# Kernel optimization log

Measured on AMD Instinct MI355X. Metric: run time of the kernel, lower is better.

The kernel has to match this reference:

```python
import jax, jax.numpy as jnp
import numpy as np

B, S, D_MODEL = 2, 2048, 2048
N_HEADS, N_KV_HEADS, HEAD_DIM = 32, 8, 64
N_GROUPS = N_HEADS // N_KV_HEADS


def setup_inputs() -> dict:
    key = jax.random.key(0)
    ks = jax.random.split(key, 5)
    x = jax.random.normal(ks[0], (B, S, D_MODEL), dtype=jnp.float32)
    wq = jax.random.normal(ks[1], (N_HEADS * HEAD_DIM, D_MODEL), dtype=jnp.float32) * 0.02
    wk = jax.random.normal(ks[2], (N_KV_HEADS * HEAD_DIM, D_MODEL), dtype=jnp.float32) * 0.02
    wv = jax.random.normal(ks[3], (N_KV_HEADS * HEAD_DIM, D_MODEL), dtype=jnp.float32) * 0.02
    wo = jax.random.normal(ks[4], (D_MODEL, N_HEADS * HEAD_DIM), dtype=jnp.float32) * 0.02
    # Rotary tables: module's apply_rope expects cos/sin of shape [S, head_dim//2]
    half = HEAD_DIM // 2
    inv_freq = 1.0 / (10000.0 ** (jnp.arange(0, half, dtype=jnp.float32) / half))
    angles = jnp.arange(S, dtype=jnp.float32)[:, None] * inv_freq[None, :]  # [S, half]
    cos = jnp.cos(angles)
    sin = jnp.sin(angles)
    return {"x": x, "wq": wq, "wk": wk, "wv": wv, "wo": wo, "cos": cos, "sin": sin}


def _rotate_half(t):
    half = t.shape[-1] // 2
    return jnp.concatenate((-t[..., half:], t[..., :half]), axis=-1)


def _apply_rope(q, k, cos, sin):
    # cos/sin: [S, head_dim//2] -> repeat_interleave(2) -> [S, head_dim]
    cos2 = jnp.repeat(cos, 2, axis=-1)[None, :, None, :]  # [1,S,1,D]
    sin2 = jnp.repeat(sin, 2, axis=-1)[None, :, None, :]
    q_rot = q * cos2 + _rotate_half(q) * sin2
    k_rot = k * cos2 + _rotate_half(k) * sin2
    return q_rot, k_rot


def reference(x, wq, wk, wv, wo, cos, sin):
    b, s, _ = x.shape
    q = (x @ wq.T).reshape(b, s, N_HEADS, HEAD_DIM)
    k = (x @ wk.T).reshape(b, s, N_KV_HEADS, HEAD_DIM)
    v = (x @ wv.T).reshape(b, s, N_KV_HEADS, HEAD_DIM)
    q, k = _apply_rope(q, k, cos, sin)
    # GQA expansion: repeat_interleave along head dim
    k = jnp.repeat(k, N_GROUPS, axis=2)  # [b,s,H,D]
    v = jnp.repeat(v, N_GROUPS, axis=2)
    q = q.transpose(0, 2, 1, 3)  # [b,H,s,D]
    k = k.transpose(0, 2, 1, 3)
    v = v.transpose(0, 2, 1, 3)
    scale = HEAD_DIM ** -0.5
    scores = jnp.einsum("bhqd,bhkd->bhqk", q, k) * scale
    causal = jnp.tril(jnp.ones((s, s), dtype=bool))
    scores = jnp.where(causal[None, None], scores, jnp.finfo(scores.dtype).min)
    attn = jax.nn.softmax(scores, axis=-1)
    out = jnp.einsum("bhqk,bhkd->bhqd", attn, v)
    out = out.transpose(0, 2, 1, 3).reshape(b, s, N_HEADS * HEAD_DIM)
    return out @ wo.T
```

## Files before the change

### kernel.cpp

```cpp
#include <hip/hip_runtime.h>
#include <hip/hip_bf16.h>

#define B_   2
#define S_   2048
#define DM   2048
#define NH   32
#define NKV  8
#define HD   64
#define MROWS 4096
#define NQKV  3072

typedef __attribute__((ext_vector_type(8))) short bf16x8;
typedef __attribute__((ext_vector_type(4))) float f32x4;
typedef __attribute__((ext_vector_type(16))) float f32x16;

__device__ __forceinline__ unsigned short f2b(float f) {
  __hip_bfloat16 h = __float2bfloat16(f);
  return *reinterpret_cast<unsigned short*>(&h);
}

__device__ __forceinline__ void gload16(const void* g, void* l) {
  __builtin_amdgcn_global_load_lds((__attribute__((address_space(1))) void*)g,
                                   (__attribute__((address_space(3))) void*)l,
                                   16, 0, 0);
}

__device__ __forceinline__ unsigned cvtpk(float lo, float hi) {
  unsigned r;
  asm("v_cvt_pk_bf16_f32 %0, %1, %2" : "=v"(r) : "v"(lo), "v"(hi));
  return r;
}

__device__ __forceinline__ void pl32swap(unsigned& a, unsigned& b) {
  asm volatile("v_permlane32_swap_b32 %0, %1" : "+v"(a), "+v"(b));
}

__device__ __forceinline__ float exp2hw(float x) {
  float r;
  asm("v_exp_f32 %0, %1" : "=v"(r) : "v"(x));
  return r;
}

__device__ __forceinline__ bf16x8 mk8(unsigned w0, unsigned w1, unsigned w2, unsigned w3) {
  union { unsigned u[4]; bf16x8 v; } uu;
  uu.u[0] = w0; uu.u[1] = w1; uu.u[2] = w2; uu.u[3] = w3;
  return uu.v;
}

__global__ __launch_bounds__(256) void f2bf_kernel(const float* __restrict__ in,
                                                   unsigned short* __restrict__ out, int n4) {
  int i = blockIdx.x * 256 + threadIdx.x;
  if (i < n4) {
    float4 v = reinterpret_cast<const float4*>(in)[i];
    ushort4 o;
    o.x = f2b(v.x); o.y = f2b(v.y); o.z = f2b(v.z); o.w = f2b(v.w);
    reinterpret_cast<ushort4*>(out)[i] = o;
  }
}

__global__ __launch_bounds__(256) void wcat_kernel(const float* __restrict__ wq,
                                                   const float* __restrict__ wk,
                                                   const float* __restrict__ wv,
                                                   unsigned short* __restrict__ out) {
  int i = blockIdx.x * 256 + threadIdx.x;
  int e = i * 4;
  int row = e >> 11;
  int col = e & 2047;
  const float* src;
  if (row < 2048)      src = wq + (size_t)row * 2048 + col;
  else if (row < 2560) src = wk + (size_t)(row - 2048) * 2048 + col;
  else                 src = wv + (size_t)(row - 2560) * 2048 + col;
  float4 v = *reinterpret_cast<const float4*>(src);
  ushort4 o;
  o.x = f2b(v.x); o.y = f2b(v.y); o.z = f2b(v.z); o.w = f2b(v.w);
  reinterpret_cast<ushort4*>(out)[i] = o;
}

#define QSCALE 0.18033688011112042f

__global__ __launch_bounds__(256, 3) void gemm_qkv(const unsigned short* __restrict__ A,
                                                   const unsigned short* __restrict__ Bm,
                                                   unsigned short* __restrict__ Qb,
                                                   unsigned short* __restrict__ Kb2,
                                                   unsigned short* __restrict__ Vtb,
                                                   const float* __restrict__ cosg,
                                                   const float* __restrict__ sing) {
  const int K = DM;
  __shared__ unsigned short Abuf[3][128 * 32];
  __shared__ unsigned short Bbuf[3][128 * 32];
  const int tid = threadIdx.x;
  const int wave = tid >> 6, lane = tid & 63;
  const int wr = wave >> 1, wc = wave & 1;
  const int rowbase = blockIdx.y * 128;
  const int colbase = blockIdx.x * 128;
  const unsigned short* Ag = A + (size_t)rowbase * K;
  const unsigned short* Bg = Bm + (size_t)colbase * K;
  const int NT = K / 32;

  auto stage = [&](int buf, int k0) {
#pragma unroll
    for (int it = 0; it < 2; ++it) {
      int slot = wave * 128 + it * 64 + lane;
      int r = slot >> 2, p = slot & 3;
      gload16(Ag + (size_t)r * K + k0 + ((p ^ ((r >> 1) & 3)) << 3),
              &Abuf[buf][(wave * 128 + it * 64) * 8]);
    }
#pragma unroll
    for (int it = 0; it < 2; ++it) {
      int slot = wave * 128 + it * 64 + lane;
      int r = slot >> 2, p = slot & 3;
      gload16(Bg + (size_t)r * K + k0 + ((p ^ ((r >> 1) & 3)) << 3),
              &Bbuf[buf][(wave * 128 + it * 64) * 8]);
    }
  };
  auto ldA = [&](int buf, int row, int c) -> bf16x8 {
    return *(const bf16x8*)((const char*)&Abuf[buf][0] + row * 64 + ((c ^ ((row >> 1) & 3)) << 4));
  };
  auto ldB = [&](int buf, int row, int c) -> bf16x8 {
    return *(const bf16x8*)((const char*)&Bbuf[buf][0] + row * 64 + ((c ^ ((row >> 1) & 3)) << 4));
  };

  f32x4 acc[4][4];
#pragma unroll
  for (int a = 0; a < 4; a++)
#pragma unroll
    for (int b2 = 0; b2 < 4; b2++) acc[a][b2] = (f32x4){0.f, 0.f, 0.f, 0.f};

  const int l15 = lane & 15, l4 = lane >> 4;

  stage(0, 0);
  stage(1, 32);
  asm volatile("s_waitcnt vmcnt(4)" ::: "memory");
  __builtin_amdgcn_s_barrier();

  int cur = 0;
  for (int t = 0; t < NT; ++t) {
    const int nxt2 = (cur >= 1) ? cur - 1 : cur + 2;
    bf16x8 af[4], bfv[4];
#pragma unroll
    for (int mt = 0; mt < 4; ++mt) af[mt] = ldA(cur, wr * 64 + mt * 16 + l15, l4);
#pragma unroll
    for (int nt = 0; nt < 4; ++nt) bfv[nt] = ldB(cur, wc * 64 + nt * 16 + l15, l4);
    if (t + 2 < NT) stage(nxt2, (t + 2) * 32);
    __builtin_amdgcn_s_barrier();
    __builtin_amdgcn_s_setprio(1);
#pragma unroll
    for (int mt = 0; mt < 4; ++mt)
#pragma unroll
      for (int nt = 0; nt < 4; ++nt)
        acc[mt][nt] = __builtin_amdgcn_mfma_f32_16x16x32_bf16(af[mt], bfv[nt], acc[mt][nt], 0, 0, 0);
    __builtin_amdgcn_s_setprio(0);
    if (t < NT - 1) {
      if (t + 2 < NT) asm volatile("s_waitcnt vmcnt(4)" ::: "memory");
      else            asm volatile("s_waitcnt vmcnt(0)" ::: "memory");
      __builtin_amdgcn_s_barrier();
    }
    cur = (cur < 2) ? cur + 1 : 0;
  }

  const int orow = rowbase + wr * 64, ocol = colbase + wc * 64;
  if (colbase < 2048) {
#pragma unroll
    for (int mt = 0; mt < 4; ++mt)
#pragma unroll
      for (int r = 0; r < 4; ++r) {
        const int row = orow + mt * 16 + l4 * 4 + r;
        const int s = row & 2047;
        const float* cR = cosg + s * 32;
        const float* sR = sing + s * 32;
#pragma unroll
        for (int nt = 0; nt < 2; ++nt) {
          const int i2 = nt * 8 + (l15 >> 1);
          float c0 = cR[i2], sv0 = sR[i2], c1 = cR[16 + i2], sv1 = sR[16 + i2];
          float alo = acc[mt][nt][r], ahi = acc[mt][nt + 2][r];
          size_t base = (size_t)row * 2048 + ocol + nt * 16 + l15;
          Qb[base]      = f2b((alo * c0 - ahi * sv0) * QSCALE);
          Qb[base + 32] = f2b((ahi * c1 + alo * sv1) * QSCALE);
        }
      }
  } else if (colbase < 2560) {
    const int kcol = ocol - 2048;
#pragma unroll
    for (int mt = 0; mt < 4; ++mt)
#pragma unroll
      for (int r = 0; r < 4; ++r) {
        const int row = orow + mt * 16 + l4 * 4 + r;
        const int s = row & 2047;
        const float* cR = cosg + s * 32;
        const float* sR = sing + s * 32;
#pragma unroll
        for (int nt = 0; nt < 2; ++nt) {
          const int i2 = nt * 8 + (l15 >> 1);
          float c0 = cR[i2], sv0 = sR[i2], c1 = cR[16 + i2], sv1 = sR[16 + i2];
          float alo = acc[mt][nt][r], ahi = acc[mt][nt + 2][r];
          size_t base = (size_t)row * 512 + kcol + nt * 16 + l15;
          Kb2[base]      = f2b(alo * c0 - ahi * sv0);
          Kb2[base + 32] = f2b(ahi * c1 + alo * sv1);
        }
      }
  } else {
    const int hkv = (ocol - 2560) >> 6;
#pragma unroll
    for (int mt = 0; mt < 4; ++mt)
#pragma unroll
      for (int nt = 0; nt < 4; ++nt) {
        const int d = nt * 16 + l15;
        const int row0 = orow + mt * 16 + l4 * 4;
        const int b = row0 >> 11, s0i = row0 & 2047;
        ushort4 u;
        u.x = f2b(acc[mt][nt][0]); u.y = f2b(acc[mt][nt][1]);
        u.z = f2b(acc[mt][nt][2]); u.w = f2b(acc[mt][nt][3]);
        *(ushort4*)(Vtb + ((size_t)(b * NKV + hkv) * HD + d) * S_ + s0i) = u;
      }
  }
}

#define BMg 256
#define BNg 128
#define BKg 64
__global__ __launch_bounds__(512, 2) void gemm_bt(const unsigned short* __restrict__ A,
                                                  const unsigned short* __restrict__ Bm,
                                                  float* __restrict__ C,
                                                  int M, int N, int K) {
  __shared__ unsigned short Abuf[3][BMg * BKg];
  __shared__ unsigned short Bbuf[3][BNg * BKg];
  const int tid = threadIdx.x;
  const int wave = tid >> 6, lane = tid & 63;
  const int wr = wave >> 1, wc = wave & 1;
  const int rowbase = blockIdx.y * BMg;
  const int colbase = blockIdx.x * BNg;
  const unsigned short* Ag = A + (size_t)rowbase * K;
  const unsigned short* Bg = Bm + (size_t)colbase * K;
  const int NT = K / BKg;

  auto stage_half = [&](int buf, int k0, int half) {
#pragma unroll
    for (int i = 0; i < 2; ++i) {
      int c = wave * 256 + (half * 2 + i) * 64 + lane;
      int r = c >> 3, p = c & 7;
      gload16(Ag + (size_t)r * K + k0 + ((p ^ (r & 7)) << 3),
              &Abuf[buf][(wave * 256 + (half * 2 + i) * 64) * 8]);
    }
    int c = wave * 128 + half * 64 + lane;
    int r = c >> 3, p = c & 7;
    gload16(Bg + (size_t)r * K + k0 + ((p ^ (r & 7)) << 3),
            &Bbuf[buf][(wave * 128 + half * 64) * 8]);
  };
  auto ldA = [&](int buf, int row, int c16) -> bf16x8 {
    return *(const bf16x8*)((const char*)&Abuf[buf][0] + row * 128 + ((c16 ^ (row & 7)) << 4));
  };
  auto ldB = [&](int buf, int row, int c16) -> bf16x8 {
    return *(const bf16x8*)((const char*)&Bbuf[buf][0] + row * 128 + ((c16 ^ (row & 7)) << 4));
  };

  f32x4 acc[4][4];
#pragma unroll
  for (int a = 0; a < 4; a++)
#pragma unroll
    for (int b2 = 0; b2 < 4; b2++) acc[a][b2] = (f32x4){0.f, 0.f, 0.f, 0.f};

  const int l15 = lane & 15, l4 = lane >> 4;

  stage_half(0, 0, 0); stage_half(0, 0, 1);
  stage_half(1, BKg, 0); stage_half(1, BKg, 1);
  asm volatile("s_waitcnt vmcnt(6)" ::: "memory");
  __builtin_amdgcn_s_barrier();

  int cur = 0;
  for (int t = 0; t < NT; ++t) {
    const int nxt2 = (cur >= 1) ? cur - 1 : cur + 2;
    {
      bf16x8 af[4], bfv[4];
#pragma unroll
      for (int mt = 0; mt < 4; ++mt) af[mt] = ldA(cur, wr * 64 + mt * 16 + l15, l4);
#pragma unroll
      for (int nt = 0; nt < 4; ++nt) bfv[nt] = ldB(cur, wc * 64 + nt * 16 + l15, l4);
      if (t + 2 < NT) stage_half(nxt2, (t + 2) * BKg, 0);
      __builtin_amdgcn_s_barrier();
      __builtin_amdgcn_s_setprio(1);
#pragma unroll
      for (int mt = 0; mt < 4; ++mt)
#pragma unroll
        for (int nt = 0; nt < 4; ++nt)
          acc[mt][nt] = __builtin_amdgcn_mfma_f32_16x16x32_bf16(af[mt], bfv[nt], acc[mt][nt], 0, 0, 0);
      __builtin_amdgcn_s_setprio(0);
      __builtin_amdgcn_s_barrier();
    }
    {
      bf16x8 af[4], bfv[4];
#pragma unroll
      for (int mt = 0; mt < 4; ++mt) af[mt] = ldA(cur, wr * 64 + mt * 16 + l15, 4 + l4);
#pragma unroll
      for (int nt = 0; nt < 4; ++nt) bfv[nt] = ldB(cur, wc * 64 + nt * 16 + l15, 4 + l4);
      if (t + 2 < NT) stage_half(nxt2, (t + 2) * BKg, 1);
      __builtin_amdgcn_s_barrier();
      __builtin_amdgcn_s_setprio(1);
#pragma unroll
      for (int mt = 0; mt < 4; ++mt)
#pragma unroll
        for (int nt = 0; nt < 4; ++nt)
          acc[mt][nt] = __builtin_amdgcn_mfma_f32_16x16x32_bf16(af[mt], bfv[nt], acc[mt][nt], 0, 0, 0);
      __builtin_amdgcn_s_setprio(0);
      if (t < NT - 1) {
        if (t + 2 < NT) asm volatile("s_waitcnt vmcnt(6)" ::: "memory");
        else            asm volatile("s_waitcnt vmcnt(0)" ::: "memory");
        __builtin_amdgcn_s_barrier();
      }
    }
    cur = (cur < 2) ? cur + 1 : 0;
  }

  const int orow = rowbase + wr * 64, ocol = colbase + wc * 64;
#pragma unroll
  for (int mt = 0; mt < 4; mt++)
#pragma unroll
    for (int nt = 0; nt < 4; nt++)
#pragma unroll
      for (int r = 0; r < 4; r++)
        C[(size_t)(orow + mt * 16 + l4 * 4 + r) * N + ocol + nt * 16 + l15] = acc[mt][nt][r];
}

__global__ __launch_bounds__(256, 2) void attn_kernel(const unsigned short* __restrict__ Qb,
                                                      const unsigned short* __restrict__ Kb2,
                                                      const unsigned short* __restrict__ Vt,
                                                      unsigned short* __restrict__ AO) {
  const int pr = blockIdx.x, h = blockIdx.y, b = blockIdx.z;
  const int hk = h >> 2;
  __shared__ unsigned short Kbuf[2][8192];
  __shared__ unsigned short Vbuf[2][8192];
  const int tid = threadIdx.x, wave = tid >> 6, lane = tid & 63;
  const int l31 = lane & 31, hi = lane >> 5;

  const unsigned short* Qrow = Qb + (size_t)b * S_ * 2048 + h * 64;
  const unsigned short* Krow = Kb2 + (size_t)b * S_ * 512 + hk * 64;
  const unsigned short* Vbase = Vt + (size_t)(b * NKV + hk) * HD * S_;

  const int NT_A = 16 - pr;
  const int NTtot = 17;

  auto j0_of = [&](int tl) { return (tl < NT_A ? tl : tl - NT_A) * 128; };
  auto stage = [&](int j0, int bufi) {
#pragma unroll
    for (int it = 0; it < 4; ++it) {
      int slot = (wave * 4 + it) * 64 + lane;
      int row = slot >> 3, p = slot & 7;
      gload16(Krow + (size_t)(j0 + row) * 512 + ((p ^ (row & 7)) << 3),
              &Kbuf[bufi][(wave * 4 + it) * 512]);
    }
#pragma unroll
    for (int it = 0; it < 4; ++it) {
      int slot = (wave * 4 + it) * 64 + lane;
      int row = slot >> 4, p = slot & 15;
      gload16(Vbase + (size_t)row * S_ + j0 + ((p ^ (row & 15)) << 3),
              &Vbuf[bufi][(wave * 4 + it) * 512]);
    }
  };

  stage(j0_of(0), 0);
  stage(j0_of(1), 1);
  asm volatile("s_waitcnt vmcnt(8)" ::: "memory");
  __builtin_amdgcn_s_barrier();

  int cur = 0, tlin = 0;

  for (int rg = 0; rg < 2; ++rg) {
    const int qbi = rg == 0 ? (15 - pr) : pr;
    const int qb = qbi * 128;
    const int NT = qbi + 1;
    const int q0w = qb + wave * 32;
    const int qg = q0w + l31;

    bf16x8 qf[4];
#pragma unroll
    for (int c = 0; c < 4; ++c)
      qf[c] = *reinterpret_cast<const bf16x8*>(Qrow + (size_t)qg * 2048 + c * 16 + hi * 8);

    f32x16 Oa0 = {}, Oa1 = {};
    float m_old = -INFINITY, lsum = 0.f;

    for (int t = 0; t < NT; ++t, ++tlin) {
      const int j0 = t * 128;

      if (j0 < q0w + 32) {
        const char* Klc = (const char*)&Kbuf[cur][0];
        const char* Vlc = (const char*)&Vbuf[cur][0];

        f32x16 s0 = {}, s1 = {}, s2 = {}, s3 = {};
        __builtin_amdgcn_s_setprio(1);
#pragma unroll
        for (int c = 0; c < 4; ++c) {
          const int xb = ((c << 1) + hi) ^ (l31 & 7);
          bf16x8 kf0 = *(const bf16x8*)(Klc + (l31) * 128       + (xb << 4));
          s0 = __builtin_amdgcn_mfma_f32_32x32x16_bf16(kf0, qf[c], s0, 0, 0, 0);
          bf16x8 kf1 = *(const bf16x8*)(Klc + (32 + l31) * 128  + (xb << 4));
          s1 = __builtin_amdgcn_mfma_f32_32x32x16_bf16(kf1, qf[c], s1, 0, 0, 0);
          bf16x8 kf2 = *(const bf16x8*)(Klc + (64 + l31) * 128  + (xb << 4));
          s2 = __builtin_amdgcn_mfma_f32_32x32x16_bf16(kf2, qf[c], s2, 0, 0, 0);
          bf16x8 kf3 = *(const bf16x8*)(Klc + (96 + l31) * 128  + (xb << 4));
          s3 = __builtin_amdgcn_mfma_f32_32x32x16_bf16(kf3, qf[c], s3, 0, 0, 0);
        }
        __builtin_amdgcn_s_setprio(0);

        if (j0 + 127 > q0w) {
          const int kb0 = j0 + 4 * hi, kb1 = kb0 + 32, kb2m = kb0 + 64, kb3 = kb0 + 96;
#pragma unroll
          for (int r = 0; r < 16; ++r) {
            const int ko = (r & 3) + 8 * (r >> 2);
            if (kb0 + ko > qg) s0[r] = -INFINITY;
            if (kb1 + ko > qg) s1[r] = -INFINITY;
            if (kb2m + ko > qg) s2[r] = -INFINITY;
            if (kb3 + ko > qg) s3[r] = -INFINITY;
          }
        }

        float a0 = fmaxf(fmaxf(s0[0], s1[0]), fmaxf(s2[0], s3[0]));
        float a1 = fmaxf(fmaxf(s0[1], s1[1]), fmaxf(s2[1], s3[1]));
        float a2 = fmaxf(fmaxf(s0[2], s1[2]), fmaxf(s2[2], s3[2]));
        float a3 = fmaxf(fmaxf(s0[3], s1[3]), fmaxf(s2[3], s3[3]));
#pragma unroll
        for (int r = 4; r < 16; r += 4) {
          a0 = fmaxf(a0, fmaxf(fmaxf(s0[r], s1[r]), fmaxf(s2[r], s3[r])));
          a1 = fmaxf(a1, fmaxf(fmaxf(s0[r + 1], s1[r + 1]), fmaxf(s2[r + 1], s3[r + 1])));
          a2 = fmaxf(a2, fmaxf(fmaxf(s0[r + 2], s1[r + 2]), fmaxf(s2[r + 2], s3[r + 2])));
          a3 = fmaxf(a3, fmaxf(fmaxf(s0[r + 3], s1[r + 3]), fmaxf(s2[r + 3], s3[r + 3])));
        }
        float mxt = fmaxf(fmaxf(a0, a1), fmaxf(a2, a3));
        mxt = fmaxf(mxt, __shfl_xor(mxt, 32, 64));

        if (!__all(mxt - m_old <= 8.f)) {
          float mnew = fmaxf(m_old, mxt);
          float corr = exp2hw(m_old - mnew);
          m_old = mnew;
          lsum *= corr;
#pragma unroll
          for (int r = 0; r < 16; ++r) { Oa0[r] *= corr; Oa1[r] *= corr; }
        }

        float t0 = 0.f, t1 = 0.f, t2 = 0.f, t3 = 0.f;
#pragma unroll
        for (int r = 0; r < 16; r += 4) {
          s0[r]     = exp2hw(s0[r] - m_old);     t0 += s0[r];
          s0[r + 1] = exp2hw(s0[r + 1] - m_old); t1 += s0[r + 1];
          s0[r + 2] = exp2hw(s0[r + 2] - m_old); t2 += s0[r + 2];
          s0[r + 3] = exp2hw(s0[r + 3] - m_old); t3 += s0[r + 3];
        }
#pragma unroll
        for (int r = 0; r < 16; r += 4) {
          s1[r]     = exp2hw(s1[r] - m_old);     t0 += s1[r];
          s1[r + 1] = exp2hw(s1[r + 1] - m_old); t1 += s1[r + 1];
          s1[r + 2] = exp2hw(s1[r + 2] - m_old); t2 += s1[r + 2];
          s1[r + 3] = exp2hw(s1[r + 3] - m_old); t3 += s1[r + 3];
        }
#pragma unroll
        for (int r = 0; r < 16; r += 4) {
          s2[r]     = exp2hw(s2[r] - m_old);     t0 += s2[r];
          s2[r + 1] = exp2hw(s2[r + 1] - m_old); t1 += s2[r + 1];
          s2[r + 2] = exp2hw(s2[r + 2] - m_old); t2 += s2[r + 2];
          s2[r + 3] = exp2hw(s2[r + 3] - m_old); t3 += s2[r + 3];
        }
#pragma unroll
        for (int r = 0; r < 16; r += 4) {
          s3[r]     = exp2hw(s3[r] - m_old);     t0 += s3[r];
          s3[r + 1] = exp2hw(s3[r + 1] - m_old); t1 += s3[r + 1];
          s3[r + 2] = exp2hw(s3[r + 2] - m_old); t2 += s3[r + 2];
          s3[r + 3] = exp2hw(s3[r + 3] - m_old); t3 += s3[r + 3];
        }
        float rs = (t0 + t1) + (t2 + t3);
        rs += __shfl_xor(rs, 32, 64);
        lsum += rs;

        bf16x8 pf0, pf1, pf2, pf3, pf4, pf5, pf6, pf7;
        {
          unsigned aA = cvtpk(s0[0], s0[1]),  bA = cvtpk(s0[4], s0[5]);  pl32swap(aA, bA);
          unsigned aB = cvtpk(s0[2], s0[3]),  bB = cvtpk(s0[6], s0[7]);  pl32swap(aB, bB);
          pf0 = mk8(aA, aB, bA, bB);
          unsigned aC = cvtpk(s0[8], s0[9]),  bC = cvtpk(s0[12], s0[13]); pl32swap(aC, bC);
          unsigned aD = cvtpk(s0[10], s0[11]), bD = cvtpk(s0[14], s0[15]); pl32swap(aD, bD);
          pf1 = mk8(aC, aD, bC, bD);
        }
        {
          unsigned aA = cvtpk(s1[0], s1[1]),  bA = cvtpk(s1[4], s1[5]);  pl32swap(aA, bA);
          unsigned aB = cvtpk(s1[2], s1[3]),  bB = cvtpk(s1[6], s1[7]);  pl32swap(aB, bB);
          pf2 = mk8(aA, aB, bA, bB);
          unsigned aC = cvtpk(s1[8], s1[9]),  bC = cvtpk(s1[12], s1[13]); pl32swap(aC, bC);
          unsigned aD = cvtpk(s1[10], s1[11]), bD = cvtpk(s1[14], s1[15]); pl32swap(aD, bD);
          pf3 = mk8(aC, aD, bC, bD);
        }
        {
          unsigned aA = cvtpk(s2[0], s2[1]),  bA = cvtpk(s2[4], s2[5]);  pl32swap(aA, bA);
          unsigned aB = cvtpk(s2[2], s2[3]),  bB = cvtpk(s2[6], s2[7]);  pl32swap(aB, bB);
          pf4 = mk8(aA, aB, bA, bB);
          unsigned aC = cvtpk(s2[8], s2[9]),  bC = cvtpk(s2[12], s2[13]); pl32swap(aC, bC);
          unsigned aD = cvtpk(s2[10], s2[11]), bD = cvtpk(s2[14], s2[15]); pl32swap(aD, bD);
          pf5 = mk8(aC, aD, bC, bD);
        }
        {
          unsigned aA = cvtpk(s3[0], s3[1]),  bA = cvtpk(s3[4], s3[5]);  pl32swap(aA, bA);
          unsigned aB = cvtpk(s3[2], s3[3]),  bB = cvtpk(s3[6], s3[7]);  pl32swap(aB, bB);
          pf6 = mk8(aA, aB, bA, bB);
          unsigned aC = cvtpk(s3[8], s3[9]),  bC = cvtpk(s3[12], s3[13]); pl32swap(aC, bC);
          unsigned aD = cvtpk(s3[10], s3[11]), bD = cvtpk(s3[14], s3[15]); pl32swap(aD, bD);
          pf7 = mk8(aC, aD, bC, bD);
        }

        const int xv = l31 & 15;
        __builtin_amdgcn_s_setprio(1);
#define PVSTEP(PF, SK)                                                                     \
        {                                                                                  \
          const int xc = (((SK) << 1) + hi) ^ xv;                                          \
          bf16x8 vf0 = *(const bf16x8*)(Vlc + l31 * 256 + (xc << 4));                      \
          Oa0 = __builtin_amdgcn_mfma_f32_32x32x16_bf16(vf0, PF, Oa0, 0, 0, 0);            \
          bf16x8 vf1 = *(const bf16x8*)(Vlc + (32 + l31) * 256 + (xc << 4));               \
          Oa1 = __builtin_amdgcn_mfma_f32_32x32x16_bf16(vf1, PF, Oa1, 0, 0, 0);            \
        }
        PVSTEP(pf0, 0) PVSTEP(pf1, 1) PVSTEP(pf2, 2) PVSTEP(pf3, 3)
        PVSTEP(pf4, 4) PVSTEP(pf5, 5) PVSTEP(pf6, 6) PVSTEP(pf7, 7)
#undef PVSTEP
        __builtin_amdgcn_s_setprio(0);
      }

      __builtin_amdgcn_s_barrier();
      if (tlin + 2 < NTtot) stage(j0_of(tlin + 2), cur);
      if (tlin + 1 < NTtot) {
        if (tlin + 2 < NTtot) asm volatile("s_waitcnt vmcnt(8)" ::: "memory");
        else                  asm volatile("s_waitcnt vmcnt(0)" ::: "memory");
        __builtin_amdgcn_s_barrier();
      }
      cur ^= 1;
    }

    const float inv = 1.0f / lsum;
    unsigned short* ob = AO + (size_t)(b * S_ + qg) * 2048 + h * 64;
#pragma unroll
    for (int c = 0; c < 4; ++c) {
      ushort4 u0, u1;
      u0.x = f2b(Oa0[4 * c] * inv);     u0.y = f2b(Oa0[4 * c + 1] * inv);
      u0.z = f2b(Oa0[4 * c + 2] * inv); u0.w = f2b(Oa0[4 * c + 3] * inv);
      u1.x = f2b(Oa1[4 * c] * inv);     u1.y = f2b(Oa1[4 * c + 1] * inv);
      u1.z = f2b(Oa1[4 * c + 2] * inv); u1.w = f2b(Oa1[4 * c + 3] * inv);
      *(ushort4*)(ob + 8 * c + 4 * hi)      = u0;
      *(ushort4*)(ob + 32 + 8 * c + 4 * hi) = u1;
    }
  }
}

extern "C" void kernel_launch(void* const* d_in, const int* in_sizes, int n_in,
                              void* d_out, int out_size, void* d_ws, size_t ws_size,
                              hipStream_t stream) {
  (void)in_sizes; (void)n_in; (void)out_size; (void)ws_size;
  const float* x    = (const float*)d_in[0];
  const float* wq   = (const float*)d_in[1];
  const float* wk   = (const float*)d_in[2];
  const float* wv   = (const float*)d_in[3];
  const float* wo   = (const float*)d_in[4];
  const float* cosg = (const float*)d_in[5];
  const float* sing = (const float*)d_in[6];

  char* ws = (char*)d_ws;
  unsigned short* xb   = (unsigned short*)(ws);
  unsigned short* wcat = (unsigned short*)(ws + 16777216);
  unsigned short* wob  = (unsigned short*)(ws + 29360128);
  unsigned short* Qb   = (unsigned short*)(ws + 37748736);
  unsigned short* Kb2  = (unsigned short*)(ws + 54525952);
  unsigned short* Vtb  = (unsigned short*)(ws + 58720256);
  unsigned short* AO   = xb;

  f2bf_kernel<<<8192, 256, 0, stream>>>(x, xb, 2097152);
  wcat_kernel<<<6144, 256, 0, stream>>>(wq, wk, wv, wcat);
  f2bf_kernel<<<4096, 256, 0, stream>>>(wo, wob, 1048576);

  gemm_qkv<<<dim3(NQKV / 128, MROWS / 128), 256, 0, stream>>>(xb, wcat, Qb, Kb2, Vtb, cosg, sing);

  attn_kernel<<<dim3(8, NH, B_), 256, 0, stream>>>(Qb, Kb2, Vtb, AO);

  gemm_bt<<<dim3(DM / BNg, MROWS / BMg), 512, 0, stream>>>(AO, wob, (float*)d_out, MROWS, DM, DM);
}
```

Baseline: 184.3 us.

## Split fused QKV GEMM into a larger-tile Q GEMM and a separate KV GEMM

```diff
diff --git a/kernel.cpp b/kernel.cpp
--- a/kernel.cpp
+++ b/kernel.cpp
@@ -78,13 +78,127 @@
 
 #define QSCALE 0.18033688011112042f
 
-__global__ __launch_bounds__(256, 3) void gemm_qkv(const unsigned short* __restrict__ A,
-                                                   const unsigned short* __restrict__ Bm,
-                                                   unsigned short* __restrict__ Qb,
-                                                   unsigned short* __restrict__ Kb2,
-                                                   unsigned short* __restrict__ Vtb,
-                                                   const float* __restrict__ cosg,
-                                                   const float* __restrict__ sing) {
+__global__ __launch_bounds__(512, 2) void gemm_q(const unsigned short* __restrict__ A,
+                                                 const unsigned short* __restrict__ Bm,
+                                                 unsigned short* __restrict__ Qb,
+                                                 const float* __restrict__ cosg,
+                                                 const float* __restrict__ sing) {
+  const int K = DM;
+  __shared__ unsigned short Abuf[3][256 * 64];
+  __shared__ unsigned short Bbuf[3][128 * 64];
+  const int tid = threadIdx.x;
+  const int wave = tid >> 6, lane = tid & 63;
+  const int wr = wave >> 1, wc = wave & 1;
+  const int rowbase = blockIdx.y * 256;
+  const int colbase = blockIdx.x * 128;
+  const unsigned short* Ag = A + (size_t)rowbase * K;
+  const unsigned short* Bg = Bm + (size_t)colbase * K;
+  const int NT = K / 64;
+
+  auto stage_half = [&](int buf, int k0, int half) {
+#pragma unroll
+    for (int i = 0; i < 2; ++i) {
+      int c = wave * 256 + (half * 2 + i) * 64 + lane;
+      int r = c >> 3, p = c & 7;
+      gload16(Ag + (size_t)r * K + k0 + ((p ^ (r & 7)) << 3),
+              &Abuf[buf][(wave * 256 + (half * 2 + i) * 64) * 8]);
+    }
+    int c = wave * 128 + half * 64 + lane;
+    int r = c >> 3, p = c & 7;
+    gload16(Bg + (size_t)r * K + k0 + ((p ^ (r & 7)) << 3),
+            &Bbuf[buf][(wave * 128 + half * 64) * 8]);
+  };
+  auto ldA = [&](int buf, int row, int c16) -> bf16x8 {
+    return *(const bf16x8*)((const char*)&Abuf[buf][0] + row * 128 + ((c16 ^ (row & 7)) << 4));
+  };
+  auto ldB = [&](int buf, int row, int c16) -> bf16x8 {
+    return *(const bf16x8*)((const char*)&Bbuf[buf][0] + row * 128 + ((c16 ^ (row & 7)) << 4));
+  };
+
+  f32x4 acc[4][4];
+#pragma unroll
+  for (int a = 0; a < 4; a++)
+#pragma unroll
+    for (int b2 = 0; b2 < 4; b2++) acc[a][b2] = (f32x4){0.f, 0.f, 0.f, 0.f};
+
+  const int l15 = lane & 15, l4 = lane >> 4;
+
+  stage_half(0, 0, 0); stage_half(0, 0, 1);
+  stage_half(1, 64, 0); stage_half(1, 64, 1);
+  asm volatile("s_waitcnt vmcnt(6)" ::: "memory");
+  __builtin_amdgcn_s_barrier();
+
+  int cur = 0;
+  for (int t = 0; t < NT; ++t) {
+    const int nxt2 = (cur >= 1) ? cur - 1 : cur + 2;
+    {
+      bf16x8 af[4], bfv[4];
+#pragma unroll
+      for (int mt = 0; mt < 4; ++mt) af[mt] = ldA(cur, wr * 64 + mt * 16 + l15, l4);
+#pragma unroll
+      for (int nt = 0; nt < 4; ++nt) bfv[nt] = ldB(cur, wc * 64 + nt * 16 + l15, l4);
+      if (t + 2 < NT) stage_half(nxt2, (t + 2) * 64, 0);
+      __builtin_amdgcn_s_barrier();
+      __builtin_amdgcn_s_setprio(1);
+#pragma unroll
+      for (int mt = 0; mt < 4; ++mt)
+#pragma unroll
+        for (int nt = 0; nt < 4; ++nt)
+          acc[mt][nt] = __builtin_amdgcn_mfma_f32_16x16x32_bf16(af[mt], bfv[nt], acc[mt][nt], 0, 0, 0);
+      __builtin_amdgcn_s_setprio(0);
+      __builtin_amdgcn_s_barrier();
+    }
+    {
+      bf16x8 af[4], bfv[4];
+#pragma unroll
+      for (int mt = 0; mt < 4; ++mt) af[mt] = ldA(cur, wr * 64 + mt * 16 + l15, 4 + l4);
+#pragma unroll
+      for (int nt = 0; nt < 4; ++nt) bfv[nt] = ldB(cur, wc * 64 + nt * 16 + l15, 4 + l4);
+      if (t + 2 < NT) stage_half(nxt2, (t + 2) * 64, 1);
+      __builtin_amdgcn_s_barrier();
+      __builtin_amdgcn_s_setprio(1);
+#pragma unroll
+      for (int mt = 0; mt < 4; ++mt)
+#pragma unroll
+        for (int nt = 0; nt < 4; ++nt)
+          acc[mt][nt] = __builtin_amdgcn_mfma_f32_16x16x32_bf16(af[mt], bfv[nt], acc[mt][nt], 0, 0, 0);
+      __builtin_amdgcn_s_setprio(0);
+      if (t < NT - 1) {
+        if (t + 2 < NT) asm volatile("s_waitcnt vmcnt(6)" ::: "memory");
+        else            asm volatile("s_waitcnt vmcnt(0)" ::: "memory");
+        __builtin_amdgcn_s_barrier();
+      }
+    }
+    cur = (cur < 2) ? cur + 1 : 0;
+  }
+
+  const int orow = rowbase + wr * 64, ocol = colbase + wc * 64;
+#pragma unroll
+  for (int mt = 0; mt < 4; ++mt)
+#pragma unroll
+    for (int r = 0; r < 4; ++r) {
+      const int row = orow + mt * 16 + l4 * 4 + r;
+      const int s = row & 2047;
+      const float* cR = cosg + s * 32;
+      const float* sR = sing + s * 32;
+#pragma unroll
+      for (int nt = 0; nt < 2; ++nt) {
+        const int i2 = nt * 8 + (l15 >> 1);
+        float c0 = cR[i2], sv0 = sR[i2], c1 = cR[16 + i2], sv1 = sR[16 + i2];
+        float alo = acc[mt][nt][r], ahi = acc[mt][nt + 2][r];
+        size_t base = (size_t)row * 2048 + ocol + nt * 16 + l15;
+        Qb[base]      = f2b((alo * c0 - ahi * sv0) * QSCALE);
+        Qb[base + 32] = f2b((ahi * c1 + alo * sv1) * QSCALE);
+      }
+    }
+}
+
+__global__ __launch_bounds__(256, 3) void gemm_kv(const unsigned short* __restrict__ A,
+                                                  const unsigned short* __restrict__ Bm,
+                                                  unsigned short* __restrict__ Kb2,
+                                                  unsigned short* __restrict__ Vtb,
+                                                  const float* __restrict__ cosg,
+                                                  const float* __restrict__ sing) {
   const int K = DM;
   __shared__ unsigned short Abuf[3][128 * 32];
   __shared__ unsigned short Bbuf[3][128 * 32];
@@ -159,7 +273,7 @@
   }
 
   const int orow = rowbase + wr * 64, ocol = colbase + wc * 64;
-  if (colbase < 2048) {
+  if (colbase < 512) {
 #pragma unroll
     for (int mt = 0; mt < 4; ++mt)
 #pragma unroll
@@ -173,33 +287,13 @@
           const int i2 = nt * 8 + (l15 >> 1);
           float c0 = cR[i2], sv0 = sR[i2], c1 = cR[16 + i2], sv1 = sR[16 + i2];
           float alo = acc[mt][nt][r], ahi = acc[mt][nt + 2][r];
-          size_t base = (size_t)row * 2048 + ocol + nt * 16 + l15;
-          Qb[base]      = f2b((alo * c0 - ahi * sv0) * QSCALE);
-          Qb[base + 32] = f2b((ahi * c1 + alo * sv1) * QSCALE);
-        }
-      }
-  } else if (colbase < 2560) {
-    const int kcol = ocol - 2048;
-#pragma unroll
-    for (int mt = 0; mt < 4; ++mt)
-#pragma unroll
-      for (int r = 0; r < 4; ++r) {
-        const int row = orow + mt * 16 + l4 * 4 + r;
-        const int s = row & 2047;
-        const float* cR = cosg + s * 32;
-        const float* sR = sing + s * 32;
-#pragma unroll
-        for (int nt = 0; nt < 2; ++nt) {
-          const int i2 = nt * 8 + (l15 >> 1);
-          float c0 = cR[i2], sv0 = sR[i2], c1 = cR[16 + i2], sv1 = sR[16 + i2];
-          float alo = acc[mt][nt][r], ahi = acc[mt][nt + 2][r];
-          size_t base = (size_t)row * 512 + kcol + nt * 16 + l15;
+          size_t base = (size_t)row * 512 + ocol + nt * 16 + l15;
           Kb2[base]      = f2b(alo * c0 - ahi * sv0);
           Kb2[base + 32] = f2b(ahi * c1 + alo * sv1);
         }
       }
   } else {
-    const int hkv = (ocol - 2560) >> 6;
+    const int hkv = (ocol - 512) >> 6;
 #pragma unroll
     for (int mt = 0; mt < 4; ++mt)
 #pragma unroll
@@ -569,7 +663,9 @@
   wcat_kernel<<<6144, 256, 0, stream>>>(wq, wk, wv, wcat);
   f2bf_kernel<<<4096, 256, 0, stream>>>(wo, wob, 1048576);
 
-  gemm_qkv<<<dim3(NQKV / 128, MROWS / 128), 256, 0, stream>>>(xb, wcat, Qb, Kb2, Vtb, cosg, sing);
+  gemm_q<<<dim3(DM / 128, MROWS / 256), 512, 0, stream>>>(xb, wcat, Qb, cosg, sing);
+  gemm_kv<<<dim3(1024 / 128, MROWS / 128), 256, 0, stream>>>(xb, wcat + (size_t)2048 * 2048,
+                                                             Kb2, Vtb, cosg, sing);
 
   attn_kernel<<<dim3(8, NH, B_), 256, 0, stream>>>(Qb, Kb2, Vtb, AO);
 
```

Result: slower. 190.6 us (+3.4%).
